# Optimization experiments

Hardware: AMD Instinct MI355X
Metric: run time of the kernel (lower is better)

## Reference

```python
import jax, jax.numpy as jnp
import numpy as np


def setup_inputs() -> dict:
    key = jax.random.key(0)
    ks = jax.random.split(key, 8)
    B, C, T, F = 2, 2, 500, 129
    H, D = 16, 100  # hidden_channels, delay
    return {
        "x_mic": jax.random.normal(ks[0], (B, C, T, F), jnp.float32),
        "x_ref": jax.random.normal(ks[1], (B, C, T, F), jnp.float32),
        "w_mic": jax.random.normal(ks[2], (H, C), jnp.float32) * 0.5,
        "b_mic": jax.random.normal(ks[3], (H,), jnp.float32) * 0.1,
        "w_ref": jax.random.normal(ks[4], (H, C), jnp.float32) * 0.5,
        "b_ref": jax.random.normal(ks[5], (H,), jnp.float32) * 0.1,
        "w_conv": jax.random.normal(ks[6], (1, H, 5, 3), jnp.float32) * 0.05,
        "b_conv": jax.random.normal(ks[7], (1,), jnp.float32) * 0.1,
        "delay": D,
    }


def reference(x_mic, x_ref, w_mic, b_mic, w_ref, b_ref, w_conv, b_conv, delay):
    # x_mic, x_ref: (B, C, T, F)
    B, C, T, F = x_mic.shape
    # 1x1 convs == per-(t,f) channel mixing
    Q = jnp.einsum('bctf,hc->bhtf', x_mic, w_mic) + b_mic[None, :, None, None]
    K = jnp.einsum('bctf,hc->bhtf', x_ref, w_ref) + b_ref[None, :, None, None]

    # unfold: zero-pad (delay-1) frames at the start of T, take sliding windows
    # window index d at output frame t maps to K[t - (delay-1) + d]
    idx = jnp.arange(T)[:, None] + jnp.arange(delay)[None, :]  # (T, delay) indices into padded T
    Kp = jnp.pad(K, ((0, 0), (0, 0), (delay - 1, 0), (0, 0)))
    Ku = Kp[:, :, idx, :]  # (B, H, T, delay, F)

    # windowed cross-correlation over frequency
    V = jnp.einsum('bhtf,bhtdf->bhtd', Q, Ku)  # (B, H, T, delay)

    # (5,3) conv, causal pad 4 along T (height), symmetric pad 1 along delay (width)
    V = jax.lax.conv_general_dilated(
        V, w_conv, window_strides=(1, 1), padding=[(4, 0), (1, 1)],
        dimension_numbers=('NCHW', 'OIHW', 'NCHW'))
    V = V + b_conv[None, :, None, None]  # (B, 1, T, delay)

    A = jax.nn.softmax(V[:, 0], axis=-1)  # (B, T, delay) attention over delays

    # unfold raw x_ref the same way and take delay-weighted sum
    Rp = jnp.pad(x_ref, ((0, 0), (0, 0), (delay - 1, 0), (0, 0)))
    Ru = Rp[:, :, idx, :]  # (B, C, T, delay, F)
    y = jnp.einsum('bctdf,btd->bctf', Ru, A)  # (B, C, T, F)
    return y
```

## Files before the change

### kernel.cpp

```cpp
#include <hip/hip_runtime.h>
#include <math.h>

constexpr int NB = 2;
constexpr int NC = 2;
constexpr int NT = 500;
constexpr int NF = 129;
constexpr int NH = 16;
constexpr int ND = 100;

constexpr int VTS = NT + 4;
constexpr int VDS = ND + 2;
constexpr size_t VELEMS = (size_t)NB * NH * VTS * VDS;

typedef _Float16 f16;
typedef _Float16 f16x4 __attribute__((ext_vector_type(4)));
typedef float    f32x4 __attribute__((ext_vector_type(4)));

constexpr int TT   = 16;
constexpr int NTT  = (NT + TT - 1) / TT;
constexpr int LROWS = 144;
constexpr int LSTR  = 148;

__global__ __launch_bounds__(256) void v_kernel(
    const float* __restrict__ x_mic, const float* __restrict__ x_ref,
    const float* __restrict__ w_mic, const float* __restrict__ b_mic,
    const float* __restrict__ w_ref, const float* __restrict__ b_ref,
    float* __restrict__ Vp)
{
    __shared__ f16 Lds[LROWS * LSTR];

    const int tid = threadIdx.x;
    const int tt  = blockIdx.x & 31;
    const int bh  = blockIdx.x >> 5;
    const int h = bh & 15, b = bh >> 4;
    const int ts = tt * TT;
    const int US = ts - (ND - 1);

    const float wm0 = w_mic[h*NC+0], wm1 = w_mic[h*NC+1], bm = b_mic[h];
    const float wr0 = w_ref[h*NC+0], wr1 = w_ref[h*NC+1], br = b_ref[h];

    const float* xm0 = x_mic + ((size_t)b*NC + 0) * NT * NF;
    const float* xm1 = x_mic + ((size_t)b*NC + 1) * NT * NF;
    const float* xr0 = x_ref + ((size_t)b*NC + 0) * NT * NF;
    const float* xr1 = x_ref + ((size_t)b*NC + 1) * NT * NF;

    const int w = tid >> 6;
    const int l = tid & 63;

    for (int rr = 0; rr < 36; ++rr) {
        const int r = w + 4 * rr;
        const bool isK = (r < 128);
        const int row = isK ? (US + r) : (ts + r - 128);
        const bool valid = (row >= 0) && (row < NT);
        const float* p0 = isK ? xr0 : xm0;
        const float* p1 = isK ? xr1 : xm1;
        const float w0 = isK ? wr0 : wm0;
        const float w1 = isK ? wr1 : wm1;
        const float bb = isK ? br  : bm;
        const size_t base = (size_t)row * NF;
        f16* ldsrow = Lds + r * LSTR;

        float v0 = 0.f, v1 = 0.f;
        if (valid) {
            v0 = w0 * p0[base + l]      + w1 * p1[base + l]      + bb;
            v1 = w0 * p0[base + l + 64] + w1 * p1[base + l + 64] + bb;
        }
        ldsrow[l]      = (f16)v0;
        ldsrow[l + 64] = (f16)v1;
        if (l < LSTR - 128) {
            const int c = 128 + l;
            float v2 = (valid && c < NF) ? (w0 * p0[base + c] + w1 * p1[base + c] + bb) : 0.f;
            ldsrow[c] = (f16)v2;
        }
    }
    __syncthreads();

    const int lr = l & 15;
    const int lk = l >> 4;
    f32x4 acc0 = {0.f, 0.f, 0.f, 0.f};
    f32x4 acc1 = {0.f, 0.f, 0.f, 0.f};

    #pragma unroll
    for (int kk = 0; kk < 9; ++kk) {
        const int fo = 16 * kk + 4 * lk;
        f16x4 a  = *(const f16x4*)&Lds[(128 + lr) * LSTR + fo];
        f16x4 b0 = *(const f16x4*)&Lds[(32*w      + lr) * LSTR + fo];
        f16x4 b1 = *(const f16x4*)&Lds[(32*w + 16 + lr) * LSTR + fo];
        acc0 = __builtin_amdgcn_mfma_f32_16x16x16f16(a, b0, acc0, 0, 0, 0);
        acc1 = __builtin_amdgcn_mfma_f32_16x16x16f16(a, b1, acc1, 0, 0, 0);
    }

    float* Vb = Vp + (size_t)bh * VTS * VDS;
    #pragma unroll
    for (int j = 0; j < 4; ++j) {
        const int t_loc = 4 * lk + j;
        const int t_g = ts + t_loc;
        if (t_g < NT) {
            const int u0 = 32*w + lr;
            const int d0 = u0 - t_loc;
            if (d0 >= 0 && d0 < ND) Vb[(size_t)(t_g + 4) * VDS + d0 + 1] = acc0[j];
            const int u1 = u0 + 16;
            const int d1 = u1 - t_loc;
            if (d1 >= 0 && d1 < ND) Vb[(size_t)(t_g + 4) * VDS + d1 + 1] = acc1[j];
        }
    }

    if (tid < 32) {
        const int rr = tid >> 1, side = tid & 1;
        const int t_g = ts + rr;
        if (t_g < NT)
            Vb[(size_t)(t_g + 4) * VDS + (side ? (VDS - 1) : 0)] = 0.f;
    }
    if (tt == 0) {
        for (int q = tid; q < 4 * VDS; q += 256) Vb[q] = 0.f;
    }
}

__global__ __launch_bounds__(256) void csy_kernel(
    const float* __restrict__ Vp, const float* __restrict__ w_conv,
    const float* __restrict__ b_conv, const float* __restrict__ x_ref,
    float* __restrict__ y)
{
    const int t = blockIdx.x % NT;
    const int b = blockIdx.x / NT;
    const int tid = threadIdx.x;
    const int d = tid;

    __shared__ float Alds[ND];
    __shared__ float red[4];

    float s = 0.f;
    if (d < ND) {
        #pragma unroll 4
        for (int h = 0; h < NH; ++h) {
            const float* Vb = Vp + ((size_t)(b*NH + h) * VTS + t) * VDS + d;
            const float* wh = w_conv + h * 15;
            #pragma unroll
            for (int kt = 0; kt < 5; ++kt)
                #pragma unroll
                for (int kd = 0; kd < 3; ++kd)
                    s += wh[kt*3 + kd] * Vb[kt*VDS + kd];
        }
        s += b_conv[0];
    }

    if (tid < 128) {
        float m = (d < ND) ? s : -3.4e38f;
        #pragma unroll
        for (int o = 32; o > 0; o >>= 1) m = fmaxf(m, __shfl_down(m, o, 64));
        if ((tid & 63) == 0) red[tid >> 6] = m;
    }
    __syncthreads();
    const float m = fmaxf(red[0], red[1]);
    const float e = (d < ND) ? __expf(s - m) : 0.f;
    if (tid < 128) {
        float sm = e;
        #pragma unroll
        for (int o = 32; o > 0; o >>= 1) sm += __shfl_down(sm, o, 64);
        if ((tid & 63) == 0) red[2 + (tid >> 6)] = sm;
    }
    __syncthreads();
    const float inv = 1.f / (red[2] + red[3]);
    if (d < ND) Alds[d] = e * inv;
    __syncthreads();

    const int d0 = (t >= ND - 1) ? 0 : (ND - 1 - t);
    for (int o = tid; o < NC * NF; o += 256) {
        const int c = o / NF, f = o - c * NF;
        const float* X = x_ref + ((size_t)(b*NC + c) * NT + (t + d0 - (ND - 1))) * NF + f;
        float acc = 0.f;
        #pragma unroll 4
        for (int dd = d0; dd < ND; ++dd) {
            acc += Alds[dd] * X[0];
            X += NF;
        }
        y[((size_t)(b*NC + c) * NT + t) * NF + f] = acc;
    }
}

extern "C" void kernel_launch(void* const* d_in, const int* in_sizes, int n_in,
                              void* d_out, int out_size, void* d_ws, size_t ws_size,
                              hipStream_t stream)
{
    const float* x_mic  = (const float*)d_in[0];
    const float* x_ref  = (const float*)d_in[1];
    const float* w_mic  = (const float*)d_in[2];
    const float* b_mic  = (const float*)d_in[3];
    const float* w_ref  = (const float*)d_in[4];
    const float* b_ref  = (const float*)d_in[5];
    const float* w_conv = (const float*)d_in[6];
    const float* b_conv = (const float*)d_in[7];
    float* y = (float*)d_out;

    float* Vp = (float*)d_ws;

    v_kernel<<<dim3(NB * NH * NTT), dim3(256), 0, stream>>>(
        x_mic, x_ref, w_mic, b_mic, w_ref, b_ref, Vp);
    csy_kernel<<<dim3(NB * NT), dim3(256), 0, stream>>>(
        Vp, w_conv, b_conv, x_ref, y);
}
```

Measured before the change: 121.0 us.

## Factor per-head correlation into nine channel-pair maps folded with conv weights

Because the 1x1 convolutions are linear, the per-head windowed correlation is rewritten as nine raw channel-pair correlation maps (mic channel or bias times ref channel or bias). The first kernel computes these maps with MFMA from raw inputs, and the second folds the head weights, biases and conv taps into a 9x15 coefficient table before applying the 5x3 convolution. This replaces 32 per-head V maps with 18 smaller ones and cuts correlation work and workspace traffic. The trade-off is extra MFMAs per block and a longer inner loop in the conv stage, and fp16 rounding now applies to raw inputs rather than to projected Q and K.

Result: faster. 108.5 us (-10.4%).

```diff
diff --git a/kernel.cpp b/kernel.cpp
--- a/kernel.cpp
+++ b/kernel.cpp
@@ -8,151 +8,164 @@
 constexpr int NH = 16;
 constexpr int ND = 100;
 
-constexpr int VTS = NT + 4;
-constexpr int VDS = ND + 2;
-constexpr size_t VELEMS = (size_t)NB * NH * VTS * VDS;
+constexpr int NMAP = 9;
+constexpr size_t CSTRIDE = (size_t)NT * ND;
+constexpr size_t CELEMS  = (size_t)NB * NMAP * CSTRIDE;
 
 typedef _Float16 f16;
 typedef _Float16 f16x4 __attribute__((ext_vector_type(4)));
 typedef float    f32x4 __attribute__((ext_vector_type(4)));
 
-constexpr int TT   = 16;
-constexpr int NTT  = (NT + TT - 1) / TT;
-constexpr int LROWS = 144;
+constexpr int TT    = 16;
+constexpr int NTT   = 32;
+constexpr int BROWS = 128;
+constexpr int LROWS = 176;
 constexpr int LSTR  = 148;
 
-__global__ __launch_bounds__(256) void v_kernel(
+__global__ __launch_bounds__(256) void corr_kernel(
     const float* __restrict__ x_mic, const float* __restrict__ x_ref,
-    const float* __restrict__ w_mic, const float* __restrict__ b_mic,
-    const float* __restrict__ w_ref, const float* __restrict__ b_ref,
-    float* __restrict__ Vp)
+    float* __restrict__ C)
 {
     __shared__ f16 Lds[LROWS * LSTR];
 
     const int tid = threadIdx.x;
-    const int tt  = blockIdx.x & 31;
-    const int bh  = blockIdx.x >> 5;
-    const int h = bh & 15, b = bh >> 4;
+    const int tt = blockIdx.x & 31;
+    const int bj = blockIdx.x >> 5;
+    const int j = bj % 3, b = bj / 3;
     const int ts = tt * TT;
     const int US = ts - (ND - 1);
 
-    const float wm0 = w_mic[h*NC+0], wm1 = w_mic[h*NC+1], bm = b_mic[h];
-    const float wr0 = w_ref[h*NC+0], wr1 = w_ref[h*NC+1], br = b_ref[h];
-
-    const float* xm0 = x_mic + ((size_t)b*NC + 0) * NT * NF;
-    const float* xm1 = x_mic + ((size_t)b*NC + 1) * NT * NF;
-    const float* xr0 = x_ref + ((size_t)b*NC + 0) * NT * NF;
-    const float* xr1 = x_ref + ((size_t)b*NC + 1) * NT * NF;
+    const float* xr = x_ref + (size_t)b * NC * NT * NF;
+    const float* xm = x_mic + (size_t)b * NC * NT * NF;
 
     const int w = tid >> 6;
     const int l = tid & 63;
 
-    for (int rr = 0; rr < 36; ++rr) {
+    for (int rr = 0; rr < 44; ++rr) {
         const int r = w + 4 * rr;
-        const bool isK = (r < 128);
-        const int row = isK ? (US + r) : (ts + r - 128);
-        const bool valid = (row >= 0) && (row < NT);
-        const float* p0 = isK ? xr0 : xm0;
-        const float* p1 = isK ? xr1 : xm1;
-        const float w0 = isK ? wr0 : wm0;
-        const float w1 = isK ? wr1 : wm1;
-        const float bb = isK ? br  : bm;
-        const size_t base = (size_t)row * NF;
-        f16* ldsrow = Lds + r * LSTR;
-
-        float v0 = 0.f, v1 = 0.f;
-        if (valid) {
-            v0 = w0 * p0[base + l]      + w1 * p1[base + l]      + bb;
-            v1 = w0 * p0[base + l + 64] + w1 * p1[base + l + 64] + bb;
-        }
-        ldsrow[l]      = (f16)v0;
-        ldsrow[l + 64] = (f16)v1;
-        if (l < LSTR - 128) {
-            const int c = 128 + l;
-            float v2 = (valid && c < NF) ? (w0 * p0[base + c] + w1 * p1[base + c] + bb) : 0.f;
-            ldsrow[c] = (f16)v2;
-        }
+        f16* row = Lds + r * LSTR;
+        float v0 = 0.f, v1 = 0.f, v2 = 0.f;
+        if (r < BROWS) {
+            const int u = US + r;
+            if (u >= 0 && u < NT) {
+                if (j < 2) {
+                    const float* p = xr + (size_t)j * NT * NF + (size_t)u * NF;
+                    v0 = p[l]; v1 = p[l + 64]; if (l == 0) v2 = p[128];
+                } else { v0 = 1.f; v1 = 1.f; if (l == 0) v2 = 1.f; }
+            }
+        } else {
+            const int q = r - BROWS;
+            const int i = q >> 4;
+            const int t = ts + (q & 15);
+            if (t < NT) {
+                if (i < 2) {
+                    const float* p = xm + (size_t)i * NT * NF + (size_t)t * NF;
+                    v0 = p[l]; v1 = p[l + 64]; if (l == 0) v2 = p[128];
+                } else { v0 = 1.f; v1 = 1.f; if (l == 0) v2 = 1.f; }
+            }
+        }
+        row[l]      = (f16)v0;
+        row[l + 64] = (f16)v1;
+        if (l < LSTR - 128) row[128 + l] = (l == 0) ? (f16)v2 : (f16)0.f;
     }
     __syncthreads();
 
     const int lr = l & 15;
     const int lk = l >> 4;
-    f32x4 acc0 = {0.f, 0.f, 0.f, 0.f};
-    f32x4 acc1 = {0.f, 0.f, 0.f, 0.f};
+    f32x4 acc[3][2] = {};
 
     #pragma unroll
     for (int kk = 0; kk < 9; ++kk) {
         const int fo = 16 * kk + 4 * lk;
-        f16x4 a  = *(const f16x4*)&Lds[(128 + lr) * LSTR + fo];
-        f16x4 b0 = *(const f16x4*)&Lds[(32*w      + lr) * LSTR + fo];
-        f16x4 b1 = *(const f16x4*)&Lds[(32*w + 16 + lr) * LSTR + fo];
-        acc0 = __builtin_amdgcn_mfma_f32_16x16x16f16(a, b0, acc0, 0, 0, 0);
-        acc1 = __builtin_amdgcn_mfma_f32_16x16x16f16(a, b1, acc1, 0, 0, 0);
-    }
-
-    float* Vb = Vp + (size_t)bh * VTS * VDS;
+        f16x4 bf0 = *(const f16x4*)&Lds[(32*w      + lr) * LSTR + fo];
+        f16x4 bf1 = *(const f16x4*)&Lds[(32*w + 16 + lr) * LSTR + fo];
+        #pragma unroll
+        for (int i = 0; i < 3; ++i) {
+            f16x4 af = *(const f16x4*)&Lds[(BROWS + 16*i + lr) * LSTR + fo];
+            acc[i][0] = __builtin_amdgcn_mfma_f32_16x16x16f16(af, bf0, acc[i][0], 0, 0, 0);
+            acc[i][1] = __builtin_amdgcn_mfma_f32_16x16x16f16(af, bf1, acc[i][1], 0, 0, 0);
+        }
+    }
+
     #pragma unroll
-    for (int j = 0; j < 4; ++j) {
-        const int t_loc = 4 * lk + j;
-        const int t_g = ts + t_loc;
-        if (t_g < NT) {
-            const int u0 = 32*w + lr;
-            const int d0 = u0 - t_loc;
-            if (d0 >= 0 && d0 < ND) Vb[(size_t)(t_g + 4) * VDS + d0 + 1] = acc0[j];
-            const int u1 = u0 + 16;
-            const int d1 = u1 - t_loc;
-            if (d1 >= 0 && d1 < ND) Vb[(size_t)(t_g + 4) * VDS + d1 + 1] = acc1[j];
-        }
-    }
-
-    if (tid < 32) {
-        const int rr = tid >> 1, side = tid & 1;
-        const int t_g = ts + rr;
-        if (t_g < NT)
-            Vb[(size_t)(t_g + 4) * VDS + (side ? (VDS - 1) : 0)] = 0.f;
-    }
-    if (tt == 0) {
-        for (int q = tid; q < 4 * VDS; q += 256) Vb[q] = 0.f;
+    for (int i = 0; i < 3; ++i) {
+        float* Cb = C + ((size_t)b * NMAP + (i*3 + j)) * CSTRIDE;
+        #pragma unroll
+        for (int n = 0; n < 2; ++n) {
+            const int u_loc = 32*w + 16*n + lr;
+            #pragma unroll
+            for (int jj = 0; jj < 4; ++jj) {
+                const int t_loc = 4*lk + jj;
+                const int t_g = ts + t_loc;
+                const int d = u_loc - t_loc;
+                if (t_g < NT && d >= 0 && d < ND)
+                    Cb[(size_t)t_g * ND + d] = acc[i][n][jj];
+            }
+        }
     }
 }
 
 __global__ __launch_bounds__(256) void csy_kernel(
-    const float* __restrict__ Vp, const float* __restrict__ w_conv,
-    const float* __restrict__ b_conv, const float* __restrict__ x_ref,
-    float* __restrict__ y)
+    const float* __restrict__ C, const float* __restrict__ w_conv,
+    const float* __restrict__ b_conv,
+    const float* __restrict__ w_mic, const float* __restrict__ b_mic,
+    const float* __restrict__ w_ref, const float* __restrict__ b_ref,
+    const float* __restrict__ x_ref, float* __restrict__ y)
 {
     const int t = blockIdx.x % NT;
     const int b = blockIdx.x / NT;
     const int tid = threadIdx.x;
-    const int d = tid;
-
+
+    __shared__ float G[NMAP][15];
     __shared__ float Alds[ND];
     __shared__ float red[4];
 
+    if (tid < NMAP * 15) {
+        const int m = tid / 15, tap = tid % 15;
+        const int i = m / 3, jj = m % 3;
+        float s = 0.f;
+        for (int h = 0; h < NH; ++h) {
+            const float a  = (i  < 2) ? w_mic[h*NC + i]  : b_mic[h];
+            const float bb = (jj < 2) ? w_ref[h*NC + jj] : b_ref[h];
+            s += w_conv[h*15 + tap] * a * bb;
+        }
+        G[m][tap] = s;
+    }
+    __syncthreads();
+
+    const int d = tid;
     float s = 0.f;
     if (d < ND) {
-        #pragma unroll 4
-        for (int h = 0; h < NH; ++h) {
-            const float* Vb = Vp + ((size_t)(b*NH + h) * VTS + t) * VDS + d;
-            const float* wh = w_conv + h * 15;
+        const float* Cb = C + (size_t)b * NMAP * CSTRIDE;
+        #pragma unroll
+        for (int kt = 0; kt < 5; ++kt) {
+            const int tp = t - 4 + kt;
+            if (tp < 0) continue;
             #pragma unroll
-            for (int kt = 0; kt < 5; ++kt)
+            for (int kd = 0; kd < 3; ++kd) {
+                const int dp = d - 1 + kd;
+                if (dp < 0 || dp >= ND) continue;
+                const float* p = Cb + (size_t)tp * ND + dp;
+                const int tap = kt*3 + kd;
+                float a2 = 0.f;
                 #pragma unroll
-                for (int kd = 0; kd < 3; ++kd)
-                    s += wh[kt*3 + kd] * Vb[kt*VDS + kd];
+                for (int m = 0; m < NMAP; ++m)
+                    a2 += G[m][tap] * p[m * CSTRIDE];
+                s += a2;
+            }
         }
         s += b_conv[0];
     }
 
     if (tid < 128) {
-        float m = (d < ND) ? s : -3.4e38f;
-        #pragma unroll
-        for (int o = 32; o > 0; o >>= 1) m = fmaxf(m, __shfl_down(m, o, 64));
-        if ((tid & 63) == 0) red[tid >> 6] = m;
-    }
-    __syncthreads();
-    const float m = fmaxf(red[0], red[1]);
-    const float e = (d < ND) ? __expf(s - m) : 0.f;
+        float mx = (d < ND) ? s : -3.4e38f;
+        #pragma unroll
+        for (int o = 32; o > 0; o >>= 1) mx = fmaxf(mx, __shfl_down(mx, o, 64));
+        if ((tid & 63) == 0) red[tid >> 6] = mx;
+    }
+    __syncthreads();
+    const float mx = fmaxf(red[0], red[1]);
+    const float e = (d < ND) ? __expf(s - mx) : 0.f;
     if (tid < 128) {
         float sm = e;
         #pragma unroll
@@ -192,10 +205,9 @@
     const float* b_conv = (const float*)d_in[7];
     float* y = (float*)d_out;
 
-    float* Vp = (float*)d_ws;
-
-    v_kernel<<<dim3(NB * NH * NTT), dim3(256), 0, stream>>>(
-        x_mic, x_ref, w_mic, b_mic, w_ref, b_ref, Vp);
+    float* C = (float*)d_ws;
+
+    corr_kernel<<<dim3(NB * 3 * NTT), dim3(256), 0, stream>>>(x_mic, x_ref, C);
     csy_kernel<<<dim3(NB * NT), dim3(256), 0, stream>>>(
-        Vp, w_conv, b_conv, x_ref, y);
+        C, w_conv, b_conv, w_mic, b_mic, w_ref, b_ref, x_ref, y);
 }
```
